# Kernel tuning notes

Hardware: AMD Instinct MI355X
Metric: run time of the kernel (lower is better)

## Reference

```python
import jax, jax.numpy as jnp
import numpy as np

B, C_IN, H, W = 8, 64, 64, 64
C_MID = 32


def setup_inputs() -> dict:
    key = jax.random.key(0)
    ks = jax.random.split(key, 7)
    s = 1.0 / np.sqrt(C_IN)
    return {
        "x": jax.random.normal(ks[0], (B, C_IN, H, W), dtype=jnp.float32),
        "Wk": jax.random.normal(ks[1], (C_MID, C_IN), dtype=jnp.float32) * s,
        "bk": jax.random.normal(ks[2], (C_MID,), dtype=jnp.float32) * 0.01,
        "Wq": jax.random.normal(ks[3], (C_MID, C_IN), dtype=jnp.float32) * s,
        "bq": jax.random.normal(ks[4], (C_MID,), dtype=jnp.float32) * 0.01,
        "Wv": jax.random.normal(ks[5], (C_MID, C_IN), dtype=jnp.float32) * s,
        "bv": jax.random.normal(ks[6], (C_MID,), dtype=jnp.float32) * 0.01,
    }


def reference(x, Wk, bk, Wq, bq, Wv, bv):
    # 1x1 convs == per-pixel channel projections
    def proj(Wt, bt):
        return jnp.einsum('bchw,oc->bohw', x, Wt) + bt[None, :, None, None]

    k = proj(Wk, bk)  # [B, Cm, H, W]
    q = proj(Wq, bq)
    v = proj(Wv, bv)

    b, c, h, w = q.shape
    n = h * w
    qf = q.reshape(b, c, n)
    kf = k.reshape(b, c, n)
    vf = v.reshape(b, c, n)

    # correlated_weight over spatial dims [2,3]: QK channel correlation per
    # pixel pair, softmax over key positions, weighted sum of V.
    scores = jnp.einsum('bcn,bcm->bnm', qf, kf)      # [B, N, N]
    attn = jax.nn.softmax(scores, axis=-1)
    out = jnp.einsum('bnm,bcm->bcn', attn, vf)       # [B, Cm, N]
    return out.reshape(b, c, h, w)
```

## Files before the change

### kernel.cpp

```cpp
#include <hip/hip_runtime.h>
#include <hip/hip_bf16.h>
#include <cstdint>
#include <cstddef>


typedef _Float16 f16x8 __attribute__((ext_vector_type(8)));
typedef float  f32x16 __attribute__((ext_vector_type(16)));
typedef float  f32x4  __attribute__((ext_vector_type(4)));

struct alignas(16) U4 { uint32_t w[4]; };
struct alignas(8)  U2 { uint32_t w[2]; };

#define MFMA16(A, B, C) __builtin_amdgcn_mfma_f32_32x32x16_f16((A), (B), (C), 0, 0, 0)

__device__ __forceinline__ uint16_t f2h(float f) {
    _Float16 h = (_Float16)f;
    return __builtin_bit_cast(uint16_t, h);
}
__device__ __forceinline__ uint16_t f2bf(float f) {
    uint32_t u = __builtin_bit_cast(uint32_t, f);
    u += 0x7fffu + ((u >> 16) & 1u);
    return (uint16_t)(u >> 16);
}
__device__ __forceinline__ float bf2f(uint32_t h16) {
    uint32_t u = h16 << 16;
    return __builtin_bit_cast(float, u);
}
__device__ __forceinline__ uint32_t cvtpk16(float lo, float hi) {
    auto h2 = __builtin_amdgcn_cvt_pkrtz(lo, hi);
    return __builtin_bit_cast(uint32_t, h2);
}
__device__ __forceinline__ void swp(uint32_t& a, uint32_t& b) {
    asm("v_permlane32_swap_b32 %0, %1" : "+v"(a), "+v"(b));
}
__device__ __forceinline__ float ex2(float x) {
    float r;
    asm("v_exp_f32 %0, %1" : "=v"(r) : "v"(x));
    return r;
}
__device__ __forceinline__ float max3(float a, float b, float c) {
    return fmaxf(fmaxf(a, b), c);
}
__device__ __forceinline__ f16x8 ld8(const void* p) {
    return __builtin_bit_cast(f16x8, *(const U4*)p);
}
__device__ __forceinline__ void gload16(const void* g, void* l) {
    __builtin_amdgcn_global_load_lds(
        (const __attribute__((address_space(1))) void*)g,
        (__attribute__((address_space(3))) void*)l, 16, 0, 0);
}

__global__ __launch_bounds__(256) void proj_kernel(
    const float* __restrict__ x,
    const float* __restrict__ Wk, const float* __restrict__ bk,
    const float* __restrict__ Wq, const float* __restrict__ bq,
    const float* __restrict__ Wv, const float* __restrict__ bv,
    uint16_t* __restrict__ qf, uint16_t* __restrict__ kf,
    uint16_t* __restrict__ vt)
{
    __shared__ __align__(16) char xtile[64 * 256];

    const int tid = threadIdx.x;
    const int blk = blockIdx.x;
    const int b   = blk >> 6;
    const int n0  = (blk & 63) << 6;
    const int wv  = __builtin_amdgcn_readfirstlane(tid >> 6);
    const int lane = tid & 63;
    const int px  = lane;
    const int n   = n0 + px;
    const int ob  = wv << 3;

    {
        const char* src = (const char*)(x + (size_t)b * 64 * 4096 + n0)
                        + ((size_t)(16 * wv + (lane >> 4))) * 16384
                        + (lane & 15) * 16;
        char* dst = xtile + wv * 4096;
        #pragma unroll
        for (int j = 0; j < 4; ++j)
            gload16(src + (size_t)(4 * j) * 16384, dst + j * 1024);
    }
    __syncthreads();

    float xv[64];
    #pragma unroll
    for (int ci = 0; ci < 64; ++ci)
        xv[ci] = *(const float*)(xtile + ci * 256 + px * 4);

    #pragma unroll
    for (int pass = 0; pass < 3; ++pass) {
        const float* W    = pass == 0 ? Wk : (pass == 1 ? Wq : Wv);
        const float* bias = pass == 0 ? bk : (pass == 1 ? bq : bv);
        float acc[8];
        #pragma unroll
        for (int o = 0; o < 8; ++o) acc[o] = bias[ob + o];
        #pragma unroll
        for (int o = 0; o < 8; ++o) {
            const float* wr = W + (size_t)(ob + o) * 64;
            #pragma unroll
            for (int ci = 0; ci < 64; ++ci)
                acc[o] = fmaf(wr[ci], xv[ci], acc[o]);
        }
        if (pass == 2) {
            #pragma unroll
            for (int o = 0; o < 8; ++o) {
                int c   = ob + o;
                int nsw = (n & ~0x38) | ((((n >> 3) & 7) ^ (c & 7)) << 3);
                vt[((size_t)(b * 32 + c)) * 4096 + nsw] = f2h(acc[o]);
            }
        } else {
            if (pass == 1) {
                #pragma unroll
                for (int o = 0; o < 8; ++o) acc[o] *= 1.44269504f;
            }
            U4 u;
            #pragma unroll
            for (int t = 0; t < 4; ++t)
                u.w[t] = (uint32_t)f2h(acc[2 * t]) | ((uint32_t)f2h(acc[2 * t + 1]) << 16);
            if (pass == 0) {
                char* rowb = (char*)kf + ((size_t)(b * 4096 + n)) * 64;
                *(U4*)(rowb + ((wv ^ (n & 3)) * 16)) = u;
            } else {
                *(U4*)(qf + ((size_t)(b * 4096 + n)) * 32 + ob) = u;
            }
        }
    }
}

__global__ __launch_bounds__(256, 4) void attn_kernel(
    const uint16_t* __restrict__ qf, const uint16_t* __restrict__ kf,
    const uint16_t* __restrict__ vt, float* __restrict__ out,
    uint16_t* __restrict__ opart, float* __restrict__ mpart,
    float* __restrict__ lpart, int ns)
{
    __shared__ __align__(16) char lds_k[2][2][4096];
    __shared__ __align__(16) char lds_v[2][2][4096];

    const int blk    = blockIdx.x;
    const int b      = blk & 7;
    const int rest   = blk >> 3;
    const int qblk   = rest & 31;
    const int ksp    = rest >> 5;
    const int ntiles = 64 / ns;
    const int kb0    = ksp * ntiles;
    const int niter  = ntiles >> 1;

    const int tid  = threadIdx.x;
    const int wv   = __builtin_amdgcn_readfirstlane(tid >> 6);
    const int lane = tid & 63;
    const int l31  = lane & 31;
    const int h32  = lane >> 5;
    const int qrow = qblk * 128 + wv * 32 + l31;

    f16x8 q0, q1;
    {
        const uint16_t* r = qf + ((size_t)(b * 4096 + qrow)) * 32;
        q0 = ld8(r + h32 * 8);
        q1 = ld8(r + 16 + h32 * 8);
    }

    f32x16 oacc, zf;
    #pragma unroll
    for (int i = 0; i < 16; ++i) { oacc[i] = 0.f; zf[i] = 0.f; }
    float m_run = -3.0e38f, l_run = 0.f;

    const char* gk   = (const char*)kf + ((size_t)b * 4096) * 64;
    const char* gv   = (const char*)vt
                     + ((size_t)(b * 32 + wv * 8 + (lane >> 3))) * 8192
                     + (lane & 7) * 16;
    const char* gk_l = gk + wv * 1024 + lane * 16;

    const int ka0 = l31 * 64 + ((h32 ^ (l31 & 3)) * 16);
    const int ka1 = l31 * 64 + (((2 + h32) ^ (l31 & 3)) * 16);
    int vo[4];
    #pragma unroll
    for (int j = 0; j < 4; ++j)
        vo[j] = l31 * 128 + (((h32 + 2 * j) ^ (l31 & 7)) * 16);

    gload16(gk_l + (size_t)kb0 * 4096,       lds_k[0][0] + wv * 1024);
    gload16(gv   + (size_t)kb0 * 128,        lds_v[0][0] + wv * 1024);
    gload16(gk_l + (size_t)(kb0 + 1) * 4096, lds_k[0][1] + wv * 1024);
    gload16(gv   + (size_t)(kb0 + 1) * 128,  lds_v[0][1] + wv * 1024);

    int p = 0;
    #pragma unroll 1
    for (int it = 0; it < niter; ++it) {
        __syncthreads();

        if (it + 1 < niter) {
            const int tn = kb0 + 2 * it + 2;
            gload16(gk_l + (size_t)tn * 4096,       lds_k[p ^ 1][0] + wv * 1024);
            gload16(gv   + (size_t)tn * 128,        lds_v[p ^ 1][0] + wv * 1024);
            gload16(gk_l + (size_t)(tn + 1) * 4096, lds_k[p ^ 1][1] + wv * 1024);
            gload16(gv   + (size_t)(tn + 1) * 128,  lds_v[p ^ 1][1] + wv * 1024);
        }

        #pragma unroll
        for (int sl = 0; sl < 2; ++sl) {
            const char* lk = lds_k[p][sl];
            const char* lv = lds_v[p][sl];

            f32x16 s0, s1;
            {
                f16x8 a0 = ld8(lk + ka0);
                f16x8 a1 = ld8(lk + ka1);
                f16x8 c0 = ld8(lk + 2048 + ka0);
                f16x8 c1 = ld8(lk + 2048 + ka1);
                s0 = MFMA16(a0, q0, zf);
                s1 = MFMA16(c0, q0, zf);
                s0 = MFMA16(a1, q1, s0);
                s1 = MFMA16(c1, q1, s1);
            }

            float mx[4];
            #pragma unroll
            for (int i = 0; i < 4; ++i)
                mx[i] = max3(max3(s0[i], s0[i + 4], s0[i + 8]),
                             max3(s0[i + 12], s1[i], s1[i + 4]),
                             fmaxf(s1[i + 8], s1[i + 12]));
            float pm = fmaxf(max3(mx[0], mx[1], mx[2]), mx[3]);
            pm = fmaxf(pm, __shfl_xor(pm, 32));

            if (__any(pm > m_run + 6.f)) {
                float mn  = fmaxf(m_run, pm);
                float scl = ex2(m_run - mn);
                l_run *= scl;
                #pragma unroll
                for (int i = 0; i < 16; ++i) oacc[i] *= scl;
                m_run = mn;
            }

            #pragma unroll
            for (int i = 0; i < 16; ++i) {
                s0[i] = ex2(s0[i] - m_run);
                s1[i] = ex2(s1[i] - m_run);
            }
            float sm[8];
            #pragma unroll
            for (int i = 0; i < 8; ++i)
                sm[i] = (s0[i] + s0[i + 8]) + (s1[i] + s1[i + 8]);
            #pragma unroll
            for (int i = 0; i < 4; ++i) sm[i] += sm[i + 4];
            float rs = (sm[0] + sm[2]) + (sm[1] + sm[3]);
            rs += __shfl_xor(rs, 32);
            l_run += rs;

            U4 f1, f2, f3, f4;
            {
                uint32_t A = cvtpk16(s0[0], s0[1]),  B = cvtpk16(s0[4], s0[5]);   swp(A, B);
                uint32_t C = cvtpk16(s0[2], s0[3]),  D = cvtpk16(s0[6], s0[7]);   swp(C, D);
                f1.w[0] = A; f1.w[1] = C; f1.w[2] = B; f1.w[3] = D;
                A = cvtpk16(s0[8], s0[9]);   B = cvtpk16(s0[12], s0[13]);  swp(A, B);
                C = cvtpk16(s0[10], s0[11]); D = cvtpk16(s0[14], s0[15]);  swp(C, D);
                f2.w[0] = A; f2.w[1] = C; f2.w[2] = B; f2.w[3] = D;
                A = cvtpk16(s1[0], s1[1]);   B = cvtpk16(s1[4], s1[5]);    swp(A, B);
                C = cvtpk16(s1[2], s1[3]);   D = cvtpk16(s1[6], s1[7]);    swp(C, D);
                f3.w[0] = A; f3.w[1] = C; f3.w[2] = B; f3.w[3] = D;
                A = cvtpk16(s1[8], s1[9]);   B = cvtpk16(s1[12], s1[13]);  swp(A, B);
                C = cvtpk16(s1[10], s1[11]); D = cvtpk16(s1[14], s1[15]);  swp(C, D);
                f4.w[0] = A; f4.w[1] = C; f4.w[2] = B; f4.w[3] = D;
            }

            {
                f16x8 v0 = ld8(lv + vo[0]);
                f16x8 v1 = ld8(lv + vo[1]);
                f16x8 v2 = ld8(lv + vo[2]);
                f16x8 v3 = ld8(lv + vo[3]);
                oacc = MFMA16(v0, __builtin_bit_cast(f16x8, f1), oacc);
                oacc = MFMA16(v1, __builtin_bit_cast(f16x8, f2), oacc);
                oacc = MFMA16(v2, __builtin_bit_cast(f16x8, f3), oacc);
                oacc = MFMA16(v3, __builtin_bit_cast(f16x8, f4), oacc);
            }
        }
        p ^= 1;
    }

    if (ns == 1) {
        const float inv = 1.f / l_run;
        float* ob = out + ((size_t)b * 32) * 4096 + qrow;
        #pragma unroll
        for (int i = 0; i < 16; ++i) {
            int c = (i & 3) + 8 * (i >> 2) + 4 * h32;
            ob[(size_t)c * 4096] = oacc[i] * inv;
        }
    } else {
        uint16_t* op = opart + ((size_t)((ksp * 8 + b) * 32)) * 4096 + qrow;
        #pragma unroll
        for (int i = 0; i < 16; ++i) {
            int c = (i & 3) + 8 * (i >> 2) + 4 * h32;
            op[(size_t)c * 4096] = f2bf(oacc[i]);
        }
        if (h32 == 0) {
            mpart[((size_t)(ksp * 8 + b)) * 4096 + qrow] = m_run;
            lpart[((size_t)(ksp * 8 + b)) * 4096 + qrow] = l_run;
        }
    }
}

__global__ __launch_bounds__(256) void reduce_kernel(
    const uint16_t* __restrict__ opart, const float* __restrict__ mpart,
    const float* __restrict__ lpart, float* __restrict__ out, int ns)
{
    const int idx = blockIdx.x * 256 + threadIdx.x;
    const int nq  = idx & 1023;
    const int c   = (idx >> 10) & 31;
    const int b   = idx >> 15;
    const size_t noff = (size_t)nq * 4;

    f32x4 M;
    #pragma unroll
    for (int e = 0; e < 4; ++e) M[e] = -3.0e38f;
    for (int s = 0; s < ns; ++s) {
        f32x4 mm = *(const f32x4*)(mpart + ((size_t)(s * 8 + b)) * 4096 + noff);
        #pragma unroll
        for (int e = 0; e < 4; ++e) M[e] = fmaxf(M[e], mm[e]);
    }
    f32x4 L, O;
    #pragma unroll
    for (int e = 0; e < 4; ++e) { L[e] = 0.f; O[e] = 0.f; }
    for (int s = 0; s < ns; ++s) {
        f32x4 mm = *(const f32x4*)(mpart + ((size_t)(s * 8 + b)) * 4096 + noff);
        f32x4 ll = *(const f32x4*)(lpart + ((size_t)(s * 8 + b)) * 4096 + noff);
        U2 uu = *(const U2*)(opart + ((size_t)((s * 8 + b) * 32 + c)) * 4096 + noff);
        float ov[4];
        ov[0] = bf2f(uu.w[0] & 0xffffu);
        ov[1] = bf2f(uu.w[0] >> 16);
        ov[2] = bf2f(uu.w[1] & 0xffffu);
        ov[3] = bf2f(uu.w[1] >> 16);
        #pragma unroll
        for (int e = 0; e < 4; ++e) {
            float w = ex2(mm[e] - M[e]);
            L[e] += ll[e] * w;
            O[e] += ov[e] * w;
        }
    }
    f32x4 r;
    #pragma unroll
    for (int e = 0; e < 4; ++e) r[e] = O[e] / L[e];
    *(f32x4*)(out + ((size_t)(b * 32 + c)) * 4096 + noff) = r;
}

extern "C" void kernel_launch(void* const* d_in, const int* in_sizes, int n_in,
                              void* d_out, int out_size, void* d_ws, size_t ws_size,
                              hipStream_t stream)
{
    (void)in_sizes; (void)n_in; (void)out_size;
    const float* x  = (const float*)d_in[0];
    const float* Wk = (const float*)d_in[1];
    const float* bk = (const float*)d_in[2];
    const float* Wq = (const float*)d_in[3];
    const float* bq = (const float*)d_in[4];
    const float* Wv = (const float*)d_in[5];
    const float* bv = (const float*)d_in[6];
    float* out = (float*)d_out;

    char* ws = (char*)d_ws;
    const size_t SZ = (size_t)8 * 4096 * 32 * 2;
    uint16_t* qf = (uint16_t*)(ws);
    uint16_t* kf = (uint16_t*)(ws + SZ);
    uint16_t* vt = (uint16_t*)(ws + 2 * SZ);
    const size_t base = 3 * SZ;

    const size_t OB  = (size_t)8 * 32 * 4096 * 2;
    const size_t MB_ = (size_t)8 * 4096 * 4;
    int ns = 1;
    if      (ws_size >= base + 4 * (OB + 2 * MB_)) ns = 4;
    else if (ws_size >= base + 2 * (OB + 2 * MB_)) ns = 2;

    uint16_t* opart = (uint16_t*)(ws + base);
    float*    mpart = (float*)(ws + base + (size_t)ns * OB);
    float*    lpart = (float*)(ws + base + (size_t)ns * OB + (size_t)ns * MB_);

    proj_kernel<<<512, 256, 0, stream>>>(x, Wk, bk, Wq, bq, Wv, bv,
                                         qf, kf, vt);
    attn_kernel<<<ns * 256, 256, 0, stream>>>(qf, kf, vt, out,
                                              opart, mpart, lpart, ns);
    if (ns > 1)
        reduce_kernel<<<1024, 256, 0, stream>>>(opart, mpart, lpart, out, ns);
}
```

Measured before the change: 60.60 us.

## Process one key tile per iteration and allow eight-way key split

The attention loop now double-buffers a single 64-key tile per stage instead of a pair of tiles, halving the LDS footprint (16KB instead of 32KB per block). This is meant to raise how many blocks fit per CU and shorten the prologue. The host also allows an 8-way key split when the workspace is large enough, which launches more blocks at the cost of a larger partial-result reduction. The trade-off is twice as many barriers per key and less work between prefetch and use.

```diff
diff --git a/kernel.cpp b/kernel.cpp
--- a/kernel.cpp
+++ b/kernel.cpp
@@ -132,8 +132,8 @@
     uint16_t* __restrict__ opart, float* __restrict__ mpart,
     float* __restrict__ lpart, int ns)
 {
-    __shared__ __align__(16) char lds_k[2][2][4096];
-    __shared__ __align__(16) char lds_v[2][2][4096];
+    __shared__ __align__(16) char lds_k[2][4096];
+    __shared__ __align__(16) char lds_v[2][4096];
 
     const int blk    = blockIdx.x;
     const int b      = blk & 7;
@@ -142,7 +142,7 @@
     const int ksp    = rest >> 5;
     const int ntiles = 64 / ns;
     const int kb0    = ksp * ntiles;
-    const int niter  = ntiles >> 1;
+    const int kb1    = kb0 + ntiles;
 
     const int tid  = threadIdx.x;
     const int wv   = __builtin_amdgcn_readfirstlane(tid >> 6);
@@ -176,102 +176,92 @@
     for (int j = 0; j < 4; ++j)
         vo[j] = l31 * 128 + (((h32 + 2 * j) ^ (l31 & 7)) * 16);
 
-    gload16(gk_l + (size_t)kb0 * 4096,       lds_k[0][0] + wv * 1024);
-    gload16(gv   + (size_t)kb0 * 128,        lds_v[0][0] + wv * 1024);
-    gload16(gk_l + (size_t)(kb0 + 1) * 4096, lds_k[0][1] + wv * 1024);
-    gload16(gv   + (size_t)(kb0 + 1) * 128,  lds_v[0][1] + wv * 1024);
-
-    int p = 0;
-    #pragma unroll 1
-    for (int it = 0; it < niter; ++it) {
+    gload16(gk_l + (size_t)kb0 * 4096, lds_k[0] + wv * 1024);
+    gload16(gv   + (size_t)kb0 * 128,  lds_v[0] + wv * 1024);
+
+    #pragma unroll 2
+    for (int kb = kb0; kb < kb1; ++kb) {
+        const int cur = kb & 1;
         __syncthreads();
 
-        if (it + 1 < niter) {
-            const int tn = kb0 + 2 * it + 2;
-            gload16(gk_l + (size_t)tn * 4096,       lds_k[p ^ 1][0] + wv * 1024);
-            gload16(gv   + (size_t)tn * 128,        lds_v[p ^ 1][0] + wv * 1024);
-            gload16(gk_l + (size_t)(tn + 1) * 4096, lds_k[p ^ 1][1] + wv * 1024);
-            gload16(gv   + (size_t)(tn + 1) * 128,  lds_v[p ^ 1][1] + wv * 1024);
-        }
-
-        #pragma unroll
-        for (int sl = 0; sl < 2; ++sl) {
-            const char* lk = lds_k[p][sl];
-            const char* lv = lds_v[p][sl];
-
-            f32x16 s0, s1;
-            {
-                f16x8 a0 = ld8(lk + ka0);
-                f16x8 a1 = ld8(lk + ka1);
-                f16x8 c0 = ld8(lk + 2048 + ka0);
-                f16x8 c1 = ld8(lk + 2048 + ka1);
-                s0 = MFMA16(a0, q0, zf);
-                s1 = MFMA16(c0, q0, zf);
-                s0 = MFMA16(a1, q1, s0);
-                s1 = MFMA16(c1, q1, s1);
-            }
-
-            float mx[4];
+        if (kb + 1 < kb1) {
+            gload16(gk_l + (size_t)(kb + 1) * 4096, lds_k[cur ^ 1] + wv * 1024);
+            gload16(gv   + (size_t)(kb + 1) * 128,  lds_v[cur ^ 1] + wv * 1024);
+        }
+
+        f32x16 s0, s1;
+        {
+            const char* lk = lds_k[cur];
+            f16x8 a0 = ld8(lk + ka0);
+            f16x8 a1 = ld8(lk + ka1);
+            f16x8 c0 = ld8(lk + 2048 + ka0);
+            f16x8 c1 = ld8(lk + 2048 + ka1);
+            s0 = MFMA16(a0, q0, zf);
+            s1 = MFMA16(c0, q0, zf);
+            s0 = MFMA16(a1, q1, s0);
+            s1 = MFMA16(c1, q1, s1);
+        }
+
+        float mx[4];
+        #pragma unroll
+        for (int i = 0; i < 4; ++i)
+            mx[i] = max3(max3(s0[i], s0[i + 4], s0[i + 8]),
+                         max3(s0[i + 12], s1[i], s1[i + 4]),
+                         fmaxf(s1[i + 8], s1[i + 12]));
+        float pm = fmaxf(max3(mx[0], mx[1], mx[2]), mx[3]);
+        pm = fmaxf(pm, __shfl_xor(pm, 32));
+
+        if (__any(pm > m_run + 6.f)) {
+            float mn  = fmaxf(m_run, pm);
+            float scl = ex2(m_run - mn);
+            l_run *= scl;
             #pragma unroll
-            for (int i = 0; i < 4; ++i)
-                mx[i] = max3(max3(s0[i], s0[i + 4], s0[i + 8]),
-                             max3(s0[i + 12], s1[i], s1[i + 4]),
-                             fmaxf(s1[i + 8], s1[i + 12]));
-            float pm = fmaxf(max3(mx[0], mx[1], mx[2]), mx[3]);
-            pm = fmaxf(pm, __shfl_xor(pm, 32));
-
-            if (__any(pm > m_run + 6.f)) {
-                float mn  = fmaxf(m_run, pm);
-                float scl = ex2(m_run - mn);
-                l_run *= scl;
-                #pragma unroll
-                for (int i = 0; i < 16; ++i) oacc[i] *= scl;
-                m_run = mn;
-            }
-
-            #pragma unroll
-            for (int i = 0; i < 16; ++i) {
-                s0[i] = ex2(s0[i] - m_run);
-                s1[i] = ex2(s1[i] - m_run);
-            }
-            float sm[8];
-            #pragma unroll
-            for (int i = 0; i < 8; ++i)
-                sm[i] = (s0[i] + s0[i + 8]) + (s1[i] + s1[i + 8]);
-            #pragma unroll
-            for (int i = 0; i < 4; ++i) sm[i] += sm[i + 4];
-            float rs = (sm[0] + sm[2]) + (sm[1] + sm[3]);
-            rs += __shfl_xor(rs, 32);
-            l_run += rs;
-
-            U4 f1, f2, f3, f4;
-            {
-                uint32_t A = cvtpk16(s0[0], s0[1]),  B = cvtpk16(s0[4], s0[5]);   swp(A, B);
-                uint32_t C = cvtpk16(s0[2], s0[3]),  D = cvtpk16(s0[6], s0[7]);   swp(C, D);
-                f1.w[0] = A; f1.w[1] = C; f1.w[2] = B; f1.w[3] = D;
-                A = cvtpk16(s0[8], s0[9]);   B = cvtpk16(s0[12], s0[13]);  swp(A, B);
-                C = cvtpk16(s0[10], s0[11]); D = cvtpk16(s0[14], s0[15]);  swp(C, D);
-                f2.w[0] = A; f2.w[1] = C; f2.w[2] = B; f2.w[3] = D;
-                A = cvtpk16(s1[0], s1[1]);   B = cvtpk16(s1[4], s1[5]);    swp(A, B);
-                C = cvtpk16(s1[2], s1[3]);   D = cvtpk16(s1[6], s1[7]);    swp(C, D);
-                f3.w[0] = A; f3.w[1] = C; f3.w[2] = B; f3.w[3] = D;
-                A = cvtpk16(s1[8], s1[9]);   B = cvtpk16(s1[12], s1[13]);  swp(A, B);
-                C = cvtpk16(s1[10], s1[11]); D = cvtpk16(s1[14], s1[15]);  swp(C, D);
-                f4.w[0] = A; f4.w[1] = C; f4.w[2] = B; f4.w[3] = D;
-            }
-
-            {
-                f16x8 v0 = ld8(lv + vo[0]);
-                f16x8 v1 = ld8(lv + vo[1]);
-                f16x8 v2 = ld8(lv + vo[2]);
-                f16x8 v3 = ld8(lv + vo[3]);
-                oacc = MFMA16(v0, __builtin_bit_cast(f16x8, f1), oacc);
-                oacc = MFMA16(v1, __builtin_bit_cast(f16x8, f2), oacc);
-                oacc = MFMA16(v2, __builtin_bit_cast(f16x8, f3), oacc);
-                oacc = MFMA16(v3, __builtin_bit_cast(f16x8, f4), oacc);
-            }
-        }
-        p ^= 1;
+            for (int i = 0; i < 16; ++i) oacc[i] *= scl;
+            m_run = mn;
+        }
+
+        #pragma unroll
+        for (int i = 0; i < 16; ++i) {
+            s0[i] = ex2(s0[i] - m_run);
+            s1[i] = ex2(s1[i] - m_run);
+        }
+        float sm[8];
+        #pragma unroll
+        for (int i = 0; i < 8; ++i)
+            sm[i] = (s0[i] + s0[i + 8]) + (s1[i] + s1[i + 8]);
+        #pragma unroll
+        for (int i = 0; i < 4; ++i) sm[i] += sm[i + 4];
+        float rs = (sm[0] + sm[2]) + (sm[1] + sm[3]);
+        rs += __shfl_xor(rs, 32);
+        l_run += rs;
+
+        U4 f1, f2, f3, f4;
+        {
+            uint32_t A = cvtpk16(s0[0], s0[1]),  B = cvtpk16(s0[4], s0[5]);   swp(A, B);
+            uint32_t C = cvtpk16(s0[2], s0[3]),  D = cvtpk16(s0[6], s0[7]);   swp(C, D);
+            f1.w[0] = A; f1.w[1] = C; f1.w[2] = B; f1.w[3] = D;
+            A = cvtpk16(s0[8], s0[9]);   B = cvtpk16(s0[12], s0[13]);  swp(A, B);
+            C = cvtpk16(s0[10], s0[11]); D = cvtpk16(s0[14], s0[15]);  swp(C, D);
+            f2.w[0] = A; f2.w[1] = C; f2.w[2] = B; f2.w[3] = D;
+            A = cvtpk16(s1[0], s1[1]);   B = cvtpk16(s1[4], s1[5]);    swp(A, B);
+            C = cvtpk16(s1[2], s1[3]);   D = cvtpk16(s1[6], s1[7]);    swp(C, D);
+            f3.w[0] = A; f3.w[1] = C; f3.w[2] = B; f3.w[3] = D;
+            A = cvtpk16(s1[8], s1[9]);   B = cvtpk16(s1[12], s1[13]);  swp(A, B);
+            C = cvtpk16(s1[10], s1[11]); D = cvtpk16(s1[14], s1[15]);  swp(C, D);
+            f4.w[0] = A; f4.w[1] = C; f4.w[2] = B; f4.w[3] = D;
+        }
+
+        {
+            const char* lv = lds_v[cur];
+            f16x8 v0 = ld8(lv + vo[0]);
+            f16x8 v1 = ld8(lv + vo[1]);
+            f16x8 v2 = ld8(lv + vo[2]);
+            f16x8 v3 = ld8(lv + vo[3]);
+            oacc = MFMA16(v0, __builtin_bit_cast(f16x8, f1), oacc);
+            oacc = MFMA16(v1, __builtin_bit_cast(f16x8, f2), oacc);
+            oacc = MFMA16(v2, __builtin_bit_cast(f16x8, f3), oacc);
+            oacc = MFMA16(v3, __builtin_bit_cast(f16x8, f4), oacc);
+        }
     }
 
     if (ns == 1) {
@@ -363,7 +353,8 @@
     const size_t OB  = (size_t)8 * 32 * 4096 * 2;
     const size_t MB_ = (size_t)8 * 4096 * 4;
     int ns = 1;
-    if      (ws_size >= base + 4 * (OB + 2 * MB_)) ns = 4;
+    if      (ws_size >= base + 8 * (OB + 2 * MB_)) ns = 8;
+    else if (ws_size >= base + 4 * (OB + 2 * MB_)) ns = 4;
     else if (ws_size >= base + 2 * (OB + 2 * MB_)) ns = 2;
 
     uint16_t* opart = (uint16_t*)(ws + base);
```

Result: slower. 72.01 us (+18.8%).
